# Optimization experiments

Hardware: AMD Instinct MI355X
Metric: run time of the kernel (lower is better)

The kernel has to match this reference:

```python
import jax, jax.numpy as jnp
import numpy as np

GROUP_SIZE = 8
OUT_FEATURES = 4096
IN_FEATURES = 4096
G = OUT_FEATURES * IN_FEATURES // GROUP_SIZE  # number of quant groups


def setup_inputs() -> dict:
    key = jax.random.key(0)
    k1, k2, k3, k4, k5 = jax.random.split(key, 5)
    x = jax.random.normal(k1, (2, 2048, IN_FEATURES), dtype=jnp.float32)
    # packed uint8 bytes, stored as int32 for harness dtype support (values 0..255)
    weight_packed = jax.random.randint(k2, (G, GROUP_SIZE // 2), 0, 256, dtype=jnp.int32)
    weight_scale = jax.random.uniform(k3, (G, 1), dtype=jnp.float32)
    weight_bias = jax.random.normal(k4, (G, 1), dtype=jnp.float32)
    bias = jax.random.normal(k5, (OUT_FEATURES,), dtype=jnp.float32)
    return {"x": x, "weight_packed": weight_packed, "weight_scale": weight_scale,
            "weight_bias": weight_bias, "bias": bias}


def dequantize_4bit(packed, scale, wbias):
    # packed: [G, gs//2] ints in [0,256); each byte holds two 4-bit values
    low = (packed & 15).astype(jnp.float32)          # even positions
    high = ((packed >> 4) & 15).astype(jnp.float32)  # odd positions
    # interleave: q[:, ::2] = low, q[:, 1::2] = high
    q = jnp.stack([low, high], axis=-1).reshape(packed.shape[0], -1)  # [G, gs]
    return q * scale + wbias  # per-group scale and bias, broadcast [G,1]->[G,gs]


def reference(x, weight_packed, weight_scale, weight_bias, bias):
    w = dequantize_4bit(weight_packed, weight_scale, weight_bias)
    w = w.reshape(OUT_FEATURES, IN_FEATURES)
    # F.linear: y = x @ w.T + bias
    return jnp.einsum('bsi,oi->bso', x, w) + bias
```

## Files before the change

### kernel.cpp

```cpp
#include <hip/hip_runtime.h>
#include <hip/hip_bf16.h>
#include <stdint.h>

#define M_DIM 4096
#define N_DIM 4096
#define K_DIM 4096
#define NGROUPS (N_DIM * K_DIM / 8)

typedef __attribute__((ext_vector_type(4))) float f32x4;
typedef __attribute__((ext_vector_type(8))) short bf16x8;
typedef __attribute__((ext_vector_type(4))) int   i32x4;

__device__ __forceinline__ ushort f2bf(float f) {
  union { float f; uint32_t u; } v; v.f = f;
  uint32_t r = v.u + 0x7FFFu + ((v.u >> 16) & 1u);
  return (ushort)(r >> 16);
}

__global__ void k_dequant_w(const int* __restrict__ wp, const float* __restrict__ wsc,
                            const float* __restrict__ wbs, ushort* __restrict__ W) {
  const int g = blockIdx.x * 256 + threadIdx.x;
  i32x4 p = *(const i32x4*)(wp + (size_t)g * 4);
  const float s = wsc[g];
  const float b = wbs[g];
  bf16x8 o;
#pragma unroll
  for (int j = 0; j < 4; ++j) {
    const float lo = (float)(p[j] & 15)        * s + b;
    const float hi = (float)((p[j] >> 4) & 15) * s + b;
    o[2 * j]     = (short)f2bf(lo);
    o[2 * j + 1] = (short)f2bf(hi);
  }
  *(bf16x8*)(W + (size_t)g * 8) = o;
}

__global__ void k_cvt_x(const float* __restrict__ x, ushort* __restrict__ X) {
  const int t = blockIdx.x * 256 + threadIdx.x;
  f32x4 a = *(const f32x4*)(x + (size_t)t * 8);
  f32x4 b = *(const f32x4*)(x + (size_t)t * 8 + 4);
  bf16x8 o;
#pragma unroll
  for (int j = 0; j < 4; ++j) {
    o[j]     = (short)f2bf(a[j]);
    o[4 + j] = (short)f2bf(b[j]);
  }
  *(bf16x8*)(X + (size_t)t * 8) = o;
}

__global__ __launch_bounds__(256) void k_gemm_bt(
    const ushort* __restrict__ A, const ushort* __restrict__ B,
    const float* __restrict__ bias, float* __restrict__ C) {
  __shared__ ushort sA[128 * 64];
  __shared__ ushort sB[128 * 64];
  const int tid  = threadIdx.x;
  const int wave = tid >> 6;
  const int lane = tid & 63;
  const int bm = blockIdx.x >> 5;
  const int bn = blockIdx.x & 31;
  const int wm = (wave >> 1) * 64;
  const int wn = (wave & 1) * 64;

  const ushort* Ab = A + (size_t)bm * 128 * K_DIM;
  const ushort* Bb = B + (size_t)bn * 128 * K_DIM;

  f32x4 acc[4][4] = {};

  const int lrow = lane & 15;
  const int lk   = (lane >> 4) * 8;

  for (int kk = 0; kk < K_DIM; kk += 64) {
#pragma unroll
    for (int i = 0; i < 4; ++i) {
      const int flat = i * 256 + tid;
      __builtin_amdgcn_global_load_lds(
          (const __attribute__((address_space(1))) void*)
              (Ab + (size_t)(flat >> 3) * K_DIM + kk + (flat & 7) * 8),
          (__attribute__((address_space(3))) void*)(sA + (i * 256 + wave * 64) * 8),
          16, 0, 0);
    }
#pragma unroll
    for (int i = 0; i < 4; ++i) {
      const int flat = i * 256 + tid;
      __builtin_amdgcn_global_load_lds(
          (const __attribute__((address_space(1))) void*)
              (Bb + (size_t)(flat >> 3) * K_DIM + kk + (flat & 7) * 8),
          (__attribute__((address_space(3))) void*)(sB + (i * 256 + wave * 64) * 8),
          16, 0, 0);
    }
    __syncthreads();

#pragma unroll
    for (int kc = 0; kc < 2; ++kc) {
      bf16x8 af[4], bq[4];
#pragma unroll
      for (int mi = 0; mi < 4; ++mi)
        af[mi] = *(const bf16x8*)(sA + (wm + mi * 16 + lrow) * 64 + kc * 32 + lk);
#pragma unroll
      for (int ni = 0; ni < 4; ++ni)
        bq[ni] = *(const bf16x8*)(sB + (wn + ni * 16 + lrow) * 64 + kc * 32 + lk);
#pragma unroll
      for (int mi = 0; mi < 4; ++mi)
#pragma unroll
        for (int ni = 0; ni < 4; ++ni)
          acc[mi][ni] = __builtin_amdgcn_mfma_f32_16x16x32_bf16(
              af[mi], bq[ni], acc[mi][ni], 0, 0, 0);
    }
    __syncthreads();
  }

  const int fr = lane & 15;
  const int fq = lane >> 4;
  const int growbase = bm * 128 + wm;
  const int gcolbase = bn * 128 + wn;
#pragma unroll
  for (int ni = 0; ni < 4; ++ni) {
    const int col = gcolbase + ni * 16 + fr;
    const float bv = bias[col];
#pragma unroll
    for (int mi = 0; mi < 4; ++mi) {
      float* cp = C + (size_t)(growbase + mi * 16 + fq * 4) * N_DIM + col;
#pragma unroll
      for (int r = 0; r < 4; ++r)
        cp[(size_t)r * N_DIM] = acc[mi][ni][r] + bv;
    }
  }
}

__global__ void k_fallback(const float* __restrict__ x, const int* __restrict__ wp,
                           const float* __restrict__ wsc, const float* __restrict__ wbs,
                           const float* __restrict__ bias, float* __restrict__ y) {
  const int m = blockIdx.x;
  const int n = blockIdx.y * 256 + threadIdx.x;
  const float* xr = x + (size_t)m * K_DIM;
  const int gbase = n * (K_DIM / 8);
  float acc = 0.f;
  for (int g = 0; g < K_DIM / 8; ++g) {
    i32x4 p = *(const i32x4*)(wp + (size_t)(gbase + g) * 4);
    const float s = wsc[gbase + g];
    const float b = wbs[gbase + g];
    const float* xk = xr + g * 8;
#pragma unroll
    for (int j = 0; j < 4; ++j) {
      acc += ((float)(p[j] & 15)        * s + b) * xk[2 * j];
      acc += ((float)((p[j] >> 4) & 15) * s + b) * xk[2 * j + 1];
    }
  }
  y[(size_t)m * N_DIM + n] = acc + bias[n];
}

extern "C" void kernel_launch(void* const* d_in, const int* in_sizes, int n_in,
                              void* d_out, int out_size, void* d_ws, size_t ws_size,
                              hipStream_t stream) {
  const float* x    = (const float*)d_in[0];
  const int*   wp   = (const int*)d_in[1];
  const float* wsc  = (const float*)d_in[2];
  const float* wbs  = (const float*)d_in[3];
  const float* bias = (const float*)d_in[4];
  float* y = (float*)d_out;

  const size_t wbytes = (size_t)N_DIM * K_DIM * sizeof(ushort);
  const size_t xbytes = (size_t)M_DIM * K_DIM * sizeof(ushort);

  if (ws_size >= wbytes + xbytes) {
    ushort* Wbf = (ushort*)d_ws;
    ushort* Xbf = (ushort*)((char*)d_ws + wbytes);
    k_dequant_w<<<NGROUPS / 256, 256, 0, stream>>>(wp, wsc, wbs, Wbf);
    k_cvt_x<<<(M_DIM * K_DIM / 8) / 256, 256, 0, stream>>>(x, Xbf);
    k_gemm_bt<<<32 * 32, 256, 0, stream>>>(Xbf, Wbf, bias, y);
  } else {
    k_fallback<<<dim3(M_DIM, N_DIM / 256), 256, 0, stream>>>(x, wp, wsc, wbs, bias, y);
  }
}
```

Baseline: 356.8 us.

## Replace GEMM with 256x256 double-buffered 8-wave kernel with swizzled LDS

Rewrites the bf16 GEMM to use 256x256 output tiles with 8 waves per block, double-buffered LDS, and XOR-swizzled shared-memory layout to avoid bank conflicts. Global-to-LDS loads for the next K tile are issued between MFMA phases, separated by barriers and s_setprio so memory traffic overlaps compute. The larger tile gives more data reuse per load but uses 128KB of LDS and many accumulator registers, which may limit occupancy. With only 256 blocks it may also leave some CUs idle.

Result: faster. 297.4 us (-16.7%).

```diff
diff --git a/kernel.cpp b/kernel.cpp
--- a/kernel.cpp
+++ b/kernel.cpp
@@ -47,77 +47,146 @@
   *(bf16x8*)(X + (size_t)t * 8) = o;
 }
 
-__global__ __launch_bounds__(256) void k_gemm_bt(
+
+#define GLD(src, dst) __builtin_amdgcn_global_load_lds(                        \
+    (const __attribute__((address_space(1))) void*)(src),                      \
+    (__attribute__((address_space(3))) void*)(dst), 16, 0, 0)
+
+__global__ __launch_bounds__(512, 2) void k_gemm_8ph(
     const ushort* __restrict__ A, const ushort* __restrict__ B,
     const float* __restrict__ bias, float* __restrict__ C) {
-  __shared__ ushort sA[128 * 64];
-  __shared__ ushort sB[128 * 64];
+  __shared__ ushort sA[2][256 * 64];
+  __shared__ ushort sB[2][256 * 64];
   const int tid  = threadIdx.x;
-  const int wave = tid >> 6;
   const int lane = tid & 63;
-  const int bm = blockIdx.x >> 5;
-  const int bn = blockIdx.x & 31;
-  const int wm = (wave >> 1) * 64;
-  const int wn = (wave & 1) * 64;
-
-  const ushort* Ab = A + (size_t)bm * 128 * K_DIM;
-  const ushort* Bb = B + (size_t)bn * 128 * K_DIM;
-
-  f32x4 acc[4][4] = {};
-
-  const int lrow = lane & 15;
-  const int lk   = (lane >> 4) * 8;
-
-  for (int kk = 0; kk < K_DIM; kk += 64) {
-#pragma unroll
-    for (int i = 0; i < 4; ++i) {
-      const int flat = i * 256 + tid;
-      __builtin_amdgcn_global_load_lds(
-          (const __attribute__((address_space(1))) void*)
-              (Ab + (size_t)(flat >> 3) * K_DIM + kk + (flat & 7) * 8),
-          (__attribute__((address_space(3))) void*)(sA + (i * 256 + wave * 64) * 8),
-          16, 0, 0);
-    }
-#pragma unroll
-    for (int i = 0; i < 4; ++i) {
-      const int flat = i * 256 + tid;
-      __builtin_amdgcn_global_load_lds(
-          (const __attribute__((address_space(1))) void*)
-              (Bb + (size_t)(flat >> 3) * K_DIM + kk + (flat & 7) * 8),
-          (__attribute__((address_space(3))) void*)(sB + (i * 256 + wave * 64) * 8),
-          16, 0, 0);
-    }
-    __syncthreads();
-
-#pragma unroll
-    for (int kc = 0; kc < 2; ++kc) {
-      bf16x8 af[4], bq[4];
-#pragma unroll
-      for (int mi = 0; mi < 4; ++mi)
-        af[mi] = *(const bf16x8*)(sA + (wm + mi * 16 + lrow) * 64 + kc * 32 + lk);
-#pragma unroll
-      for (int ni = 0; ni < 4; ++ni)
-        bq[ni] = *(const bf16x8*)(sB + (wn + ni * 16 + lrow) * 64 + kc * 32 + lk);
-#pragma unroll
-      for (int mi = 0; mi < 4; ++mi)
-#pragma unroll
-        for (int ni = 0; ni < 4; ++ni)
-          acc[mi][ni] = __builtin_amdgcn_mfma_f32_16x16x32_bf16(
-              af[mi], bq[ni], acc[mi][ni], 0, 0, 0);
-    }
+  const int wid  = tid >> 6;
+  const int wr   = wid >> 2;
+  const int wc   = wid & 3;
+  const int bm = blockIdx.x >> 4;
+  const int bn = blockIdx.x & 15;
+
+  const ushort* Ab = A + (size_t)bm * 256 * K_DIM;
+  const ushort* Bb = B + (size_t)bn * 256 * K_DIM;
+
+  const int srow = tid >> 3;
+  const int scc  = (tid & 7) ^ ((tid >> 3) & 7);
+  const int dofs = (tid >> 6) * 64 * 8;
+
+  const int l15   = lane & 15;
+  const int kx    = (lane >> 4) * 8;
+  const int xsw   = (lane & 7) << 3;
+  const int kidx0 = (0 * 32 + kx) ^ xsw;
+  const int kidx1 = (1 * 32 + kx) ^ xsw;
+  const int abase = (wr * 128 + l15) * 64;
+  const int bbase = (wc * 64 + l15) * 64;
+
+  f32x4 acc[8][4] = {};
+
+#define STAGE_A(buf, kko)                                                      \
+  _Pragma("unroll") for (int j = 0; j < 4; ++j)                                \
+      GLD(Ab + (size_t)(j * 64 + srow) * K_DIM + (kko) + scc * 8,              \
+          &sA[buf][j * 4096 + dofs]);
+#define STAGE_B(buf, kko)                                                      \
+  _Pragma("unroll") for (int j = 0; j < 4; ++j)                                \
+      GLD(Bb + (size_t)(j * 64 + srow) * K_DIM + (kko) + scc * 8,              \
+          &sB[buf][j * 4096 + dofs]);
+
+  STAGE_A(0, 0);
+  STAGE_B(0, 0);
+  __syncthreads();
+
+  for (int t = 0; t < 64; ++t) {
+    const int b  = t & 1;
+    const int kk = t * 64;
+    const ushort* sAb = sA[b];
+    const ushort* sBb = sB[b];
+    bf16x8 af[4][2], bf0[2][2], bf1[2][2];
+
+#pragma unroll
+    for (int m = 0; m < 4; ++m) {
+      af[m][0] = *(const bf16x8*)(sAb + abase + m * 1024 + kidx0);
+      af[m][1] = *(const bf16x8*)(sAb + abase + m * 1024 + kidx1);
+    }
+#pragma unroll
+    for (int n = 0; n < 2; ++n) {
+      bf0[n][0] = *(const bf16x8*)(sBb + bbase + n * 1024 + kidx0);
+      bf0[n][1] = *(const bf16x8*)(sBb + bbase + n * 1024 + kidx1);
+    }
+    if (t < 63) { STAGE_A(b ^ 1, kk + 64); }
+    __builtin_amdgcn_s_barrier();
+    __builtin_amdgcn_s_setprio(1);
+#pragma unroll
+    for (int m = 0; m < 4; ++m)
+#pragma unroll
+      for (int n = 0; n < 2; ++n)
+#pragma unroll
+        for (int kc = 0; kc < 2; ++kc)
+          acc[m][n] = __builtin_amdgcn_mfma_f32_16x16x32_bf16(
+              af[m][kc], bf0[n][kc], acc[m][n], 0, 0, 0);
+    __builtin_amdgcn_s_setprio(0);
+    __builtin_amdgcn_s_barrier();
+
+#pragma unroll
+    for (int n = 0; n < 2; ++n) {
+      bf1[n][0] = *(const bf16x8*)(sBb + bbase + (2 + n) * 1024 + kidx0);
+      bf1[n][1] = *(const bf16x8*)(sBb + bbase + (2 + n) * 1024 + kidx1);
+    }
+    if (t < 63) { STAGE_B(b ^ 1, kk + 64); }
+    __builtin_amdgcn_s_barrier();
+    __builtin_amdgcn_s_setprio(1);
+#pragma unroll
+    for (int m = 0; m < 4; ++m)
+#pragma unroll
+      for (int n = 0; n < 2; ++n)
+#pragma unroll
+        for (int kc = 0; kc < 2; ++kc)
+          acc[m][2 + n] = __builtin_amdgcn_mfma_f32_16x16x32_bf16(
+              af[m][kc], bf1[n][kc], acc[m][2 + n], 0, 0, 0);
+    __builtin_amdgcn_s_setprio(0);
+    __builtin_amdgcn_s_barrier();
+
+#pragma unroll
+    for (int m = 0; m < 4; ++m) {
+      af[m][0] = *(const bf16x8*)(sAb + abase + (4 + m) * 1024 + kidx0);
+      af[m][1] = *(const bf16x8*)(sAb + abase + (4 + m) * 1024 + kidx1);
+    }
+    __builtin_amdgcn_s_barrier();
+    __builtin_amdgcn_s_setprio(1);
+#pragma unroll
+    for (int m = 0; m < 4; ++m)
+#pragma unroll
+      for (int n = 0; n < 2; ++n)
+#pragma unroll
+        for (int kc = 0; kc < 2; ++kc)
+          acc[4 + m][2 + n] = __builtin_amdgcn_mfma_f32_16x16x32_bf16(
+              af[m][kc], bf1[n][kc], acc[4 + m][2 + n], 0, 0, 0);
+    __builtin_amdgcn_s_setprio(0);
+    __builtin_amdgcn_s_barrier();
+
+    __builtin_amdgcn_s_setprio(1);
+#pragma unroll
+    for (int m = 0; m < 4; ++m)
+#pragma unroll
+      for (int n = 0; n < 2; ++n)
+#pragma unroll
+        for (int kc = 0; kc < 2; ++kc)
+          acc[4 + m][n] = __builtin_amdgcn_mfma_f32_16x16x32_bf16(
+              af[m][kc], bf0[n][kc], acc[4 + m][n], 0, 0, 0);
+    __builtin_amdgcn_s_setprio(0);
+
     __syncthreads();
   }
 
   const int fr = lane & 15;
   const int fq = lane >> 4;
-  const int growbase = bm * 128 + wm;
-  const int gcolbase = bn * 128 + wn;
+  const int growbase = bm * 256 + wr * 128;
+  const int gcolbase = bn * 256 + wc * 64;
 #pragma unroll
   for (int ni = 0; ni < 4; ++ni) {
     const int col = gcolbase + ni * 16 + fr;
     const float bv = bias[col];
 #pragma unroll
-    for (int mi = 0; mi < 4; ++mi) {
+    for (int mi = 0; mi < 8; ++mi) {
       float* cp = C + (size_t)(growbase + mi * 16 + fq * 4) * N_DIM + col;
 #pragma unroll
       for (int r = 0; r < 4; ++r)
@@ -166,7 +235,7 @@
     ushort* Xbf = (ushort*)((char*)d_ws + wbytes);
     k_dequant_w<<<NGROUPS / 256, 256, 0, stream>>>(wp, wsc, wbs, Wbf);
     k_cvt_x<<<(M_DIM * K_DIM / 8) / 256, 256, 0, stream>>>(x, Xbf);
-    k_gemm_bt<<<32 * 32, 256, 0, stream>>>(Xbf, Wbf, bias, y);
+    k_gemm_8ph<<<16 * 16, 512, 0, stream>>>(Xbf, Wbf, bias, y);
   } else {
     k_fallback<<<dim3(M_DIM, N_DIM / 256), 256, 0, stream>>>(x, wp, wsc, wbs, bias, y);
   }
```
